# Optimization experiments

Measured on AMD Instinct MI355X. Metric: run time of the kernel, lower is better.

The kernel has to match this reference:

```python
import jax, jax.numpy as jnp
import numpy as np
from jax import lax

B, C, D, H, W = 2, 64, 16, 16, 16  # n = D*H*W = 4096; conv output length = n-2 = 4094
K = 3  # conv kernel size, dilation=2, padding=1


def setup_inputs() -> dict:
    key = jax.random.key(0)
    k1, k2, k3 = jax.random.split(key, 3)
    x = jax.random.normal(k1, (B, C, D, H, W), dtype=jnp.float32)
    # Conv1d params: weight [out_ch, in_ch, k], bias [out_ch]; PyTorch default init scale
    fan_in = C * K
    bound = 1.0 / np.sqrt(fan_in)
    conv_w = jax.random.uniform(k2, (C, C, K), jnp.float32, -bound, bound)
    conv_b = jax.random.uniform(k3, (C,), jnp.float32, -bound, bound)
    return {"x": x, "conv_w": conv_w, "conv_b": conv_b}


def _dspa(x, conv_w, conv_b):
    b, c, d, h, w = x.shape
    x1 = x.reshape(b, c, -1)  # [b, c, n]
    # dilated Conv1d: kernel=3, stride=1, padding=1, dilation=2 -> length n-2
    x2 = lax.conv_general_dilated(
        x1, conv_w,
        window_strides=(1,), padding=[(1, 1)], rhs_dilation=(2,),
        dimension_numbers=("NCH", "OIH", "NCH"),
    ) + conv_b[None, :, None]  # [b, c, n-2]
    # scores = bmm(x1^T, x2): [b, n, n-2]
    scores = jnp.einsum("bcn,bcm->bnm", x1, x2)
    # torch nn.Softmax() (dim=None) on a 3D tensor resolves to dim=0 (legacy behavior)
    x3 = jax.nn.softmax(scores, axis=0)  # [b, n, n-2]
    # x4 = bmm(x2, x3^T): [b, c, n]
    x4 = jnp.einsum("bcm,bnm->bcn", x2, x3)
    out = x1 + x4
    return out.reshape(b, c, d, h, w)


def reference(x, conv_w, conv_b):
    return _dspa(x, conv_w, conv_b)
```

## Files before the change

kernel.cpp:

```cpp
#include <hip/hip_runtime.h>

typedef unsigned short u16;
typedef unsigned int u32;
typedef __attribute__((ext_vector_type(8))) short bf16x8;
typedef __attribute__((ext_vector_type(4))) float f32x4;

#define NJ 4094

__device__ __forceinline__ u16 f2bf(float f) {
  union { float f; unsigned u; } v;
  v.f = f;
  unsigned r = v.u + 0x7fffu + ((v.u >> 16) & 1u);
  return (u16)(r >> 16);
}

__device__ __forceinline__ u32 pk_bf(float a, float b) {
  u32 ua = __float_as_uint(a) + 0x8000u;
  u32 ub = __float_as_uint(b) + 0x8000u;
  return __builtin_amdgcn_perm(ub, ua, 0x07060302u);
}

template <bool WRITE_OUT>
__global__ __launch_bounds__(256) void conv_kernel(
    const float* __restrict__ x, const float* __restrict__ w,
    const float* __restrict__ bias, u16* __restrict__ x2n, u16* __restrict__ x2T,
    float* __restrict__ out) {
  __shared__ float xs[64 * 36];
  __shared__ float wl[64 * 64 * 3];
  const int b = blockIdx.x >> 7, jt = blockIdx.x & 127;
  const int t = threadIdx.x;
  for (int idx = t; idx < 64 * 36; idx += 256) {
    int i = idx / 36, p = idx - i * 36;
    int jg = jt * 32 - 1 + p;
    float v = 0.f;
    if (jg >= 0 && jg < 4096) v = x[(b * 64 + i) * 4096 + jg];
    xs[idx] = v;
  }
  for (int idx = t; idx < 64 * 64 * 3; idx += 256) {
    int tap = idx % 3, ci = idx / 3;
    int c = ci >> 6, i = ci & 63;
    wl[(i * 64 + c) * 3 + tap] = w[idx];
  }
  __syncthreads();
  if (WRITE_OUT) {
    for (int idx = t; idx < 64 * 32; idx += 256) {
      int i = idx >> 5, k = idx & 31;
      out[(b * 64 + i) * 4096 + jt * 32 + k] = xs[i * 36 + k + 1];
    }
  }
  const int c = t & 63, jsub = t >> 6;
  float acc[8];
  float bv = bias[c];
#pragma unroll
  for (int k = 0; k < 8; k++) acc[k] = bv;
  for (int i = 0; i < 64; i++) {
    float w0 = wl[(i * 64 + c) * 3 + 0];
    float w1 = wl[(i * 64 + c) * 3 + 1];
    float w2 = wl[(i * 64 + c) * 3 + 2];
    const float* xr = &xs[i * 36 + jsub * 8];
#pragma unroll
    for (int k = 0; k < 8; k++)
      acc[k] += w0 * xr[k] + w1 * xr[k + 2] + w2 * xr[k + 4];
  }
#pragma unroll
  for (int k = 0; k < 8; k++) {
    int jg = jt * 32 + jsub * 8 + k;
    float v = (jg < NJ) ? acc[k] : 0.f;
    u16 hv = f2bf(v);
    x2n[(b * 64 + c) * 4096 + jg] = hv;
    x2T[(b * 4096 + jg) * 64 + c] = hv;
  }
}

template <bool ATOMIC>
__global__ __launch_bounds__(256, 4) void fused_kernel(
    const float* __restrict__ x, const u16* __restrict__ x2n_g,
    const u16* __restrict__ x2T_g, float* __restrict__ part_g,
    float* __restrict__ out) {
  __shared__ u16 P[2][2 * 64 * 72];
  const int t = threadIdx.x;
  const int wave = t >> 6, lane = t & 63;
  const int q = lane >> 4, ln = lane & 15;
  const int i0 = blockIdx.x * 64;
  const int jc = blockIdx.y;

  u16* xs = P[1];
#pragma unroll
  for (int rep = 0; rep < 32; rep++) {
    int idx = rep * 256 + t;
    int il = idx & 63, c = (idx >> 6) & 63, b = idx >> 12;
    float v = x[(b * 64 + c) * 4096 + i0 + il];
    if (b) v = -v;
    xs[(b * 64 + il) * 72 + c] = f2bf(v);
  }
  __syncthreads();

  bf16x8 b1[2][4][2];
#pragma unroll
  for (int b = 0; b < 2; b++)
#pragma unroll
    for (int ist = 0; ist < 4; ist++)
#pragma unroll
      for (int kc = 0; kc < 2; kc++)
        b1[b][ist][kc] = *(const bf16x8*)&xs[(b * 64 + ist * 16 + ln) * 72 + kc * 32 + q * 8];

  f32x4 acc[2][4];
#pragma unroll
  for (int a = 0; a < 2; a++)
#pragma unroll
    for (int bq = 0; bq < 4; bq++) acc[a][bq] = (f32x4){0.f, 0.f, 0.f, 0.f};

  const int b2 = wave >> 1, cs2 = (wave & 1) * 2;

  for (int jt = jc * 4; jt < jc * 4 + 4; jt++) {
    const int j0 = jt * 64;
    u16* Ps = P[jt & 1];
    f32x4 ps[4];
#pragma unroll
    for (int ist = 0; ist < 4; ist++) ps[ist] = (f32x4){0.f, 0.f, 0.f, 0.f};
#pragma unroll
    for (int b = 0; b < 2; b++)
#pragma unroll
      for (int kc = 0; kc < 2; kc++) {
        bf16x8 af = *(const bf16x8*)&x2T_g[(b * 4096 + j0 + wave * 16 + ln) * 64 + kc * 32 + q * 8];
#pragma unroll
        for (int ist = 0; ist < 4; ist++)
          ps[ist] = __builtin_amdgcn_mfma_f32_16x16x32_bf16(af, b1[b][ist][kc], ps[ist], 0, 0, 0);
      }
#pragma unroll
    for (int ist = 0; ist < 4; ist++) {
      float p0[4], p1[4];
#pragma unroll
      for (int r = 0; r < 4; r++) {
        float e = __expf(-ps[ist][r]);
        p0[r] = __builtin_amdgcn_rcpf(1.f + e);
        p1[r] = 1.f - p0[r];
      }
      uint2 o0 = make_uint2(pk_bf(p0[0], p0[1]), pk_bf(p0[2], p0[3]));
      uint2 o1 = make_uint2(pk_bf(p1[0], p1[1]), pk_bf(p1[2], p1[3]));
      *(uint2*)&Ps[(0 + ist * 16 + ln) * 72 + wave * 16 + q * 4] = o0;
      *(uint2*)&Ps[(64 + ist * 16 + ln) * 72 + wave * 16 + q * 4] = o1;
    }
    __syncthreads();
#pragma unroll
    for (int kc = 0; kc < 2; kc++) {
      bf16x8 af2[2], pb[4];
#pragma unroll
      for (int cst = 0; cst < 2; cst++)
        af2[cst] = *(const bf16x8*)&x2n_g[(b2 * 64 + (cs2 + cst) * 16 + ln) * 4096 + j0 + kc * 32 + q * 8];
#pragma unroll
      for (int ist = 0; ist < 4; ist++)
        pb[ist] = *(const bf16x8*)&Ps[(b2 * 64 + ist * 16 + ln) * 72 + kc * 32 + q * 8];
#pragma unroll
      for (int cst = 0; cst < 2; cst++)
#pragma unroll
        for (int ist = 0; ist < 4; ist++)
          acc[cst][ist] =
              __builtin_amdgcn_mfma_f32_16x16x32_bf16(af2[cst], pb[ist], acc[cst][ist], 0, 0, 0);
    }
  }
#pragma unroll
  for (int cst = 0; cst < 2; cst++)
#pragma unroll
    for (int ist = 0; ist < 4; ist++)
#pragma unroll
      for (int r = 0; r < 4; r++) {
        int c = (cs2 + cst) * 16 + q * 4 + r;
        int ii = i0 + ist * 16 + ln;
        if (ATOMIC) {
          unsafeAtomicAdd(&out[(b2 * 64 + c) * 4096 + ii], acc[cst][ist][r]);
        } else {
          part_g[(((jc * 2 + b2) * 64 + c) << 12) + ii] = acc[cst][ist][r];
        }
      }
}

__global__ __launch_bounds__(256) void reduce_kernel(
    const float4* __restrict__ x, const float4* __restrict__ part,
    float4* __restrict__ out) {
  int i = blockIdx.x * 256 + threadIdx.x;
  float4 s = x[i];
#pragma unroll
  for (int jc = 0; jc < 16; jc++) {
    float4 p = part[jc * 131072 + i];
    s.x += p.x; s.y += p.y; s.z += p.z; s.w += p.w;
  }
  out[i] = s;
}

extern "C" void kernel_launch(void* const* d_in, const int* in_sizes, int n_in,
                              void* d_out, int out_size, void* d_ws, size_t ws_size,
                              hipStream_t stream) {
  const float* x = (const float*)d_in[0];
  const float* w = (const float*)d_in[1];
  const float* bias = (const float*)d_in[2];
  float* out = (float*)d_out;
  u16* x2n = (u16*)d_ws;
  u16* x2T = x2n + 2 * 64 * 4096;
  float* part = (float*)(x2T + 2 * 64 * 4096);

  const size_t need = 2u * 64 * 4096 * 2 * 2 + 16u * 2 * 64 * 4096 * 4;
  dim3 grid(64, 16);
  if (ws_size >= need) {
    conv_kernel<false><<<256, 256, 0, stream>>>(x, w, bias, x2n, x2T, out);
    fused_kernel<false><<<grid, 256, 0, stream>>>(x, x2n, x2T, part, out);
    reduce_kernel<<<512, 256, 0, stream>>>((const float4*)x, (const float4*)part, (float4*)out);
  } else {
    conv_kernel<true><<<256, 256, 0, stream>>>(x, w, bias, x2n, x2T, out);
    fused_kernel<true><<<grid, 256, 0, stream>>>(x, x2n, x2T, nullptr, out);
  }
}
```

Baseline: 107.6 us.

## Precompute transposed bf16 x1 in conv kernel and coalesce partial stores via LDS

```diff
diff --git a/kernel.cpp b/kernel.cpp
--- a/kernel.cpp
+++ b/kernel.cpp
@@ -24,7 +24,7 @@
 __global__ __launch_bounds__(256) void conv_kernel(
     const float* __restrict__ x, const float* __restrict__ w,
     const float* __restrict__ bias, u16* __restrict__ x2n, u16* __restrict__ x2T,
-    float* __restrict__ out) {
+    u16* __restrict__ x1T, float* __restrict__ out) {
   __shared__ float xs[64 * 36];
   __shared__ float wl[64 * 64 * 3];
   const int b = blockIdx.x >> 7, jt = blockIdx.x & 127;
@@ -42,6 +42,11 @@
     wl[(i * 64 + c) * 3 + tap] = w[idx];
   }
   __syncthreads();
+  for (int idx = t; idx < 32 * 64; idx += 256) {
+    int il = idx >> 6, c = idx & 63;
+    float v = xs[c * 36 + il + 1];
+    x1T[(b * 4096 + jt * 32 + il) * 64 + c] = f2bf(b ? -v : v);
+  }
   if (WRITE_OUT) {
     for (int idx = t; idx < 64 * 32; idx += 256) {
       int i = idx >> 5, k = idx & 31;
@@ -74,7 +79,7 @@
 
 template <bool ATOMIC>
 __global__ __launch_bounds__(256, 4) void fused_kernel(
-    const float* __restrict__ x, const u16* __restrict__ x2n_g,
+    const u16* __restrict__ x1T_g, const u16* __restrict__ x2n_g,
     const u16* __restrict__ x2T_g, float* __restrict__ part_g,
     float* __restrict__ out) {
   __shared__ u16 P[2][2 * 64 * 72];
@@ -84,17 +89,6 @@
   const int i0 = blockIdx.x * 64;
   const int jc = blockIdx.y;
 
-  u16* xs = P[1];
-#pragma unroll
-  for (int rep = 0; rep < 32; rep++) {
-    int idx = rep * 256 + t;
-    int il = idx & 63, c = (idx >> 6) & 63, b = idx >> 12;
-    float v = x[(b * 64 + c) * 4096 + i0 + il];
-    if (b) v = -v;
-    xs[(b * 64 + il) * 72 + c] = f2bf(v);
-  }
-  __syncthreads();
-
   bf16x8 b1[2][4][2];
 #pragma unroll
   for (int b = 0; b < 2; b++)
@@ -102,7 +96,7 @@
     for (int ist = 0; ist < 4; ist++)
 #pragma unroll
       for (int kc = 0; kc < 2; kc++)
-        b1[b][ist][kc] = *(const bf16x8*)&xs[(b * 64 + ist * 16 + ln) * 72 + kc * 32 + q * 8];
+        b1[b][ist][kc] = *(const bf16x8*)&x1T_g[(b * 4096 + i0 + ist * 16 + ln) * 64 + kc * 32 + q * 8];
 
   f32x4 acc[2][4];
 #pragma unroll
@@ -159,20 +153,39 @@
               __builtin_amdgcn_mfma_f32_16x16x32_bf16(af2[cst], pb[ist], acc[cst][ist], 0, 0, 0);
     }
   }
-#pragma unroll
-  for (int cst = 0; cst < 2; cst++)
-#pragma unroll
-    for (int ist = 0; ist < 4; ist++)
-#pragma unroll
-      for (int r = 0; r < 4; r++) {
-        int c = (cs2 + cst) * 16 + q * 4 + r;
-        int ii = i0 + ist * 16 + ln;
-        if (ATOMIC) {
+  if (ATOMIC) {
+#pragma unroll
+    for (int cst = 0; cst < 2; cst++)
+#pragma unroll
+      for (int ist = 0; ist < 4; ist++)
+#pragma unroll
+        for (int r = 0; r < 4; r++) {
+          int c = (cs2 + cst) * 16 + q * 4 + r;
+          int ii = i0 + ist * 16 + ln;
           unsafeAtomicAdd(&out[(b2 * 64 + c) * 4096 + ii], acc[cst][ist][r]);
-        } else {
-          part_g[(((jc * 2 + b2) * 64 + c) << 12) + ii] = acc[cst][ist][r];
         }
-      }
+  } else {
+    __syncthreads();
+    float* scr = (float*)P;
+#pragma unroll
+    for (int cst = 0; cst < 2; cst++)
+#pragma unroll
+      for (int ist = 0; ist < 4; ist++)
+#pragma unroll
+        for (int r = 0; r < 4; r++) {
+          int c = (cs2 + cst) * 16 + q * 4 + r;
+          scr[(b2 * 64 + c) * 68 + ist * 16 + ln] = acc[cst][ist][r];
+        }
+    __syncthreads();
+#pragma unroll
+    for (int rep = 0; rep < 8; rep++) {
+      int idx = rep * 256 + t;
+      int crow = idx >> 4, il4 = idx & 15;
+      float4 v = *(float4*)&scr[crow * 68 + il4 * 4];
+      int b = crow >> 6, c = crow & 63;
+      *(float4*)&part_g[(((jc * 2 + b) * 64 + c) << 12) + i0 + il4 * 4] = v;
+    }
+  }
 }
 
 __global__ __launch_bounds__(256) void reduce_kernel(
@@ -197,16 +210,17 @@
   float* out = (float*)d_out;
   u16* x2n = (u16*)d_ws;
   u16* x2T = x2n + 2 * 64 * 4096;
-  float* part = (float*)(x2T + 2 * 64 * 4096);
-
-  const size_t need = 2u * 64 * 4096 * 2 * 2 + 16u * 2 * 64 * 4096 * 4;
+  u16* x1T = x2T + 2 * 64 * 4096;
+  float* part = (float*)(x1T + 2 * 64 * 4096);
+
+  const size_t need = 3u * (2 * 64 * 4096 * 2) + 16u * 2 * 64 * 4096 * 4;
   dim3 grid(64, 16);
   if (ws_size >= need) {
-    conv_kernel<false><<<256, 256, 0, stream>>>(x, w, bias, x2n, x2T, out);
-    fused_kernel<false><<<grid, 256, 0, stream>>>(x, x2n, x2T, part, out);
+    conv_kernel<false><<<256, 256, 0, stream>>>(x, w, bias, x2n, x2T, x1T, out);
+    fused_kernel<false><<<grid, 256, 0, stream>>>(x1T, x2n, x2T, part, out);
     reduce_kernel<<<512, 256, 0, stream>>>((const float4*)x, (const float4*)part, (float4*)out);
   } else {
-    conv_kernel<true><<<256, 256, 0, stream>>>(x, w, bias, x2n, x2T, out);
-    fused_kernel<true><<<grid, 256, 0, stream>>>(x, x2n, x2T, nullptr, out);
-  }
-}
+    conv_kernel<true><<<256, 256, 0, stream>>>(x, w, bias, x2n, x2T, x1T, out);
+    fused_kernel<true><<<grid, 256, 0, stream>>>(x1T, x2n, x2T, nullptr, out);
+  }
+}
```

New measurement: 109.9 us. 2.1% more time.
